# Kernel tuning notes

Hardware: AMD Instinct MI355X
Metric: run time of the kernel (lower is better)

Reference implementation:

```python
import jax, jax.numpy as jnp
import numpy as np

B, T, D, H = 4, 2048, 1024, 16
HD = D // H  # head dim = 64


def setup_inputs() -> dict:
    key = jax.random.key(0)
    ks = jax.random.split(key, 12)
    s = 1.0 / np.sqrt(D)
    inp = {
        "Q": jax.random.normal(ks[0], (B, T, D), jnp.float32),
        "K": jax.random.normal(ks[1], (B, T, D), jnp.float32),
        "V": jax.random.normal(ks[2], (B, T, D), jnp.float32),
        "mask": jnp.tril(jnp.ones((T, T), jnp.int32))[None, None],  # causal [1,1,T,T]
        "Wq": jax.random.normal(ks[3], (D, D), jnp.float32) * s,
        "bq": jax.random.normal(ks[4], (D,), jnp.float32) * s,
        "Wk": jax.random.normal(ks[5], (D, D), jnp.float32) * s,
        "bk": jax.random.normal(ks[6], (D,), jnp.float32) * s,
        "Wv": jax.random.normal(ks[7], (D, D), jnp.float32) * s,
        "bv": jax.random.normal(ks[8], (D,), jnp.float32) * s,
        "Wo": jax.random.normal(ks[9], (D, D), jnp.float32) * s,
        "bo": jax.random.normal(ks[10], (D,), jnp.float32) * s,
    }
    return inp


def reference(Q, K, V, mask, Wq, bq, Wk, bk, Wv, bv, Wo, bo):
    b, t, d = Q.shape
    # projections (torch Linear: x @ W^T + b)
    q = (Q @ Wq.T + bq).reshape(b, t, H, HD).transpose(0, 2, 1, 3)  # [b,h,t,hd]
    k = (K @ Wk.T + bk).reshape(b, t, H, HD).transpose(0, 2, 1, 3)
    v = (V @ Wv.T + bv).reshape(b, t, H, HD).transpose(0, 2, 1, 3)
    score = jnp.einsum("bhqd,bhkd->bhqk", q, k) / jnp.sqrt(jnp.float32(HD))
    score = jnp.where(mask == 0, jnp.float32(-1e9), score)
    attn = jax.nn.softmax(score, axis=-1)
    out = jnp.einsum("bhqk,bhkd->bhqd", attn, v)
    out = out.transpose(0, 2, 1, 3).reshape(b, t, d)
    return out @ Wo.T + bo
```

## Files before the change

kernel.cpp:

```cpp
#include <hip/hip_runtime.h>
#include <stdint.h>

#define B_SZ  4
#define T_SEQ 2048
#define DIM   1024
#define NH    16
#define HD    64
#define M_TOT (B_SZ * T_SEQ)

typedef unsigned short u16;
typedef unsigned long long u64;
typedef __attribute__((ext_vector_type(8))) __bf16 bf16x8;
typedef __attribute__((ext_vector_type(4))) float  floatx4;

#define SCL_Q (0.125f * 1.44269504089f)

__device__ __forceinline__ u16 f2bf(float f) {
  union { float f; uint32_t u; } v; v.f = f;
  uint32_t r = v.u + 0x7fffu + ((v.u >> 16) & 1u);
  return (u16)(r >> 16);
}

__device__ __forceinline__ void gl_lds16(const void* g, void* l) {
  __builtin_amdgcn_global_load_lds(
      (const __attribute__((address_space(1))) uint32_t*)g,
      (__attribute__((address_space(3))) uint32_t*)l, 16, 0, 0);
}

__global__ __launch_bounds__(256) void cvt_all(
    const float* __restrict__ s0, const float* __restrict__ s1,
    const float* __restrict__ s2, const float* __restrict__ s3,
    const float* __restrict__ s4, const float* __restrict__ s5,
    const float* __restrict__ s6,
    u16* __restrict__ d0, u16* __restrict__ d1, u16* __restrict__ d2,
    u16* __restrict__ d3, u16* __restrict__ d4, u16* __restrict__ d5,
    u16* __restrict__ d6) {
  const float* s; u16* d; int n;
  switch (blockIdx.y) {
    case 0: s = s0; d = d0; n = DIM * DIM; break;
    case 1: s = s1; d = d1; n = DIM * DIM; break;
    case 2: s = s2; d = d2; n = DIM * DIM; break;
    case 3: s = s3; d = d3; n = DIM * DIM; break;
    case 4: s = s4; d = d4; n = M_TOT * DIM; break;
    case 5: s = s5; d = d5; n = M_TOT * DIM; break;
    default: s = s6; d = d6; n = M_TOT * DIM; break;
  }
  int i = (blockIdx.x * 256 + threadIdx.x) * 8;
  if (i >= n) return;
  float4 a = *(const float4*)(s + i);
  float4 b = *(const float4*)(s + i + 4);
  uint4 o;
  o.x = (uint32_t)f2bf(a.x) | ((uint32_t)f2bf(a.y) << 16);
  o.y = (uint32_t)f2bf(a.z) | ((uint32_t)f2bf(a.w) << 16);
  o.z = (uint32_t)f2bf(b.x) | ((uint32_t)f2bf(b.y) << 16);
  o.w = (uint32_t)f2bf(b.z) | ((uint32_t)f2bf(b.w) << 16);
  *(uint4*)(d + i) = o;
}

#define BKG 64
__global__ __launch_bounds__(256) void gemm_qkv(
    const u16* __restrict__ Qb, const u16* __restrict__ Kb,
    const u16* __restrict__ Vb,
    const u16* __restrict__ Wq, const u16* __restrict__ Wk,
    const u16* __restrict__ Wv,
    const float* __restrict__ bq, const float* __restrict__ bk,
    const float* __restrict__ bv,
    u16* __restrict__ qo, u16* __restrict__ ko, u16* __restrict__ vo) {
  const u16* A; const u16* Bw; const float* bias; u16* Co;
  if (blockIdx.z == 0)      { A = Qb; Bw = Wq; bias = bq; Co = qo; }
  else if (blockIdx.z == 1) { A = Kb; Bw = Wk; bias = bk; Co = ko; }
  else                      { A = Vb; Bw = Wv; bias = bv; Co = vo; }

  __shared__ u16 As[128 * 64];
  __shared__ u16 Bs[128 * 64];

  const int tid  = threadIdx.x;
  const int wave = tid >> 6, lane = tid & 63;
  const int quad = lane >> 4, l16 = lane & 15;
  const int wm = wave >> 1, wn = wave & 1;
  const int m0 = blockIdx.x * 128, n0 = blockIdx.y * 128;

  const floatx4 FZ = {0.f, 0.f, 0.f, 0.f};
  floatx4 acc[4][4];
#pragma unroll
  for (int mt = 0; mt < 4; ++mt)
#pragma unroll
    for (int nt = 0; nt < 4; ++nt) acc[mt][nt] = FZ;

  for (int k0 = 0; k0 < DIM; k0 += BKG) {
    __syncthreads();
#pragma unroll
    for (int j = 0; j < 4; ++j) {
      int pc = j * 256 + tid;
      int r = pc >> 3, c = pc & 7;
      int sc = c ^ (r & 7);
      gl_lds16(A  + (size_t)(m0 + r) * DIM + k0 + sc * 8,
               &As[(j * 256 + wave * 64) * 8]);
      gl_lds16(Bw + (size_t)(n0 + r) * DIM + k0 + sc * 8,
               &Bs[(j * 256 + wave * 64) * 8]);
    }
    __syncthreads();

#pragma unroll
    for (int kk = 0; kk < 2; ++kk) {
      bf16x8 af[4], bfr[4];
#pragma unroll
      for (int mt = 0; mt < 4; ++mt) {
        int ra = wm * 64 + mt * 16 + l16;
        af[mt] = *(const bf16x8*)&As[ra * 64 + (((kk * 4 + quad) ^ (ra & 7)) * 8)];
      }
#pragma unroll
      for (int nt = 0; nt < 4; ++nt) {
        int rb = wn * 64 + nt * 16 + l16;
        bfr[nt] = *(const bf16x8*)&Bs[rb * 64 + (((kk * 4 + quad) ^ (rb & 7)) * 8)];
      }
#pragma unroll
      for (int mt = 0; mt < 4; ++mt)
#pragma unroll
        for (int nt = 0; nt < 4; ++nt)
          acc[mt][nt] = __builtin_amdgcn_mfma_f32_16x16x32_bf16(
              af[mt], bfr[nt], acc[mt][nt], 0, 0, 0);
    }
  }

  if (blockIdx.z == 2) {
#pragma unroll
    for (int nt = 0; nt < 4; ++nt) {
      int n = n0 + wn * 64 + nt * 16 + l16;
      float bb = bias[n];
      int h = n >> 6, hd = n & 63;
#pragma unroll
      for (int mt = 0; mt < 4; ++mt) {
        int mbase = m0 + wm * 64 + mt * 16 + quad * 4;
        int b = mbase >> 11, t = mbase & (T_SEQ - 1);
        u64 pk = 0;
#pragma unroll
        for (int r = 0; r < 4; ++r)
          pk |= (u64)f2bf(acc[mt][nt][r] + bb) << (16 * r);
        *(u64*)&Co[((size_t)((b * NH + h) * HD + hd)) * T_SEQ + t] = pk;
      }
    }
  } else {
    const float sc = (blockIdx.z == 0) ? SCL_Q : 1.0f;
#pragma unroll
    for (int nt = 0; nt < 4; ++nt) {
      int n = n0 + wn * 64 + nt * 16 + l16;
      float bb = bias[n];
      int h = n >> 6, hd = n & 63;
#pragma unroll
      for (int mt = 0; mt < 4; ++mt) {
#pragma unroll
        for (int r = 0; r < 4; ++r) {
          int m = m0 + wm * 64 + mt * 16 + quad * 4 + r;
          int b = m >> 11, t = m & (T_SEQ - 1);
          Co[((size_t)(b * NH + h) * T_SEQ + t) * HD + hd] =
              f2bf((acc[mt][nt][r] + bb) * sc);
        }
      }
    }
  }
}

__global__ __launch_bounds__(256) void flash_attn(
    const u16* __restrict__ qp, const u16* __restrict__ kp,
    const u16* __restrict__ vp, u16* __restrict__ ao) {
  const int bh = blockIdx.x;
  const int qt = 31 - blockIdx.y;
  const int b = bh >> 4, h = bh & 15;
  const u16* Qg = qp + (size_t)bh * T_SEQ * HD + qt * 64 * HD;
  const u16* Kg = kp + (size_t)bh * T_SEQ * HD;
  const u16* Vg = vp + (size_t)bh * HD * T_SEQ;

  __shared__ u16 lds[4][64 * 64];

  const int tid = threadIdx.x, wave = tid >> 6, lane = tid & 63;
  const int quad = lane >> 4, l16 = lane & 15;
  const int lr8 = lane >> 3, lc8 = lane & 7;

#pragma unroll
  for (int i = 0; i < 2; ++i) {
    int r = i * 32 + wave * 8 + lr8;
    int sc = lc8 ^ (r & 7);
    gl_lds16(Qg + r * 64 + sc * 8, &lds[0][(i * 32 + wave * 8) * 64]);
  }
  __syncthreads();
  bf16x8 bq_[2];
#pragma unroll
  for (int kk = 0; kk < 2; ++kk) {
    int row = wave * 16 + l16;
    int pc = (kk * 4 + quad) ^ (row & 7);
    bq_[kk] = *(const bf16x8*)&lds[0][row * 64 + pc * 8];
  }
  __syncthreads();

  const floatx4 FZ = {0.f, 0.f, 0.f, 0.f};
  floatx4 acco[4];
#pragma unroll
  for (int mt = 0; mt < 4; ++mt) acco[mt] = FZ;
  float l_p = 0.f;

  const int nkb = qt + 1;
  {
#pragma unroll
    for (int i = 0; i < 2; ++i) {
      int r = i * 32 + wave * 8 + lr8;
      int sc = lc8 ^ (r & 7);
      gl_lds16(Kg + r * 64 + sc * 8, &lds[0][(i * 32 + wave * 8) * 64]);
      gl_lds16(Vg + (size_t)r * T_SEQ + sc * 8, &lds[1][(i * 32 + wave * 8) * 64]);
    }
  }

  int p = 0;
  for (int kb = 0; kb < nkb; ++kb) {
    __syncthreads();
    if (kb + 1 < nkb) {
      const u16* Kgk = Kg + (kb + 1) * 64 * HD;
      const u16* Vgk = Vg + (kb + 1) * 64;
#pragma unroll
      for (int i = 0; i < 2; ++i) {
        int r = i * 32 + wave * 8 + lr8;
        int sc = lc8 ^ (r & 7);
        gl_lds16(Kgk + r * 64 + sc * 8, &lds[(p ^ 1) * 2][(i * 32 + wave * 8) * 64]);
        gl_lds16(Vgk + (size_t)r * T_SEQ + sc * 8,
                 &lds[(p ^ 1) * 2 + 1][(i * 32 + wave * 8) * 64]);
      }
    }
    const u16* Ks = &lds[p * 2][0];
    const u16* Vt = &lds[p * 2 + 1][0];

    floatx4 s[4];
#pragma unroll
    for (int mt = 0; mt < 4; ++mt) s[mt] = FZ;
#pragma unroll
    for (int kk = 0; kk < 2; ++kk)
#pragma unroll
      for (int mt = 0; mt < 4; ++mt) {
        int row = mt * 16 + l16;
        bf16x8 ak = *(const bf16x8*)
            &Ks[row * 64 + (((kk * 4 + quad) ^ (l16 & 7)) * 8)];
        s[mt] = __builtin_amdgcn_mfma_f32_16x16x32_bf16(ak, bq_[kk], s[mt], 0, 0, 0);
      }

    if (kb == qt) {
      int qr = wave * 16 + l16;
#pragma unroll
      for (int mt = 0; mt < 4; ++mt)
#pragma unroll
        for (int r = 0; r < 4; ++r) {
          int kvr = mt * 16 + quad * 4 + r;
          if (kvr > qr) s[mt][r] = -3e38f;
        }
    }

    float rs = 0.f;
#pragma unroll
    for (int mt = 0; mt < 4; ++mt)
#pragma unroll
      for (int r = 0; r < 4; ++r) {
        float pv_ = __builtin_amdgcn_exp2f(s[mt][r]);
        s[mt][r] = pv_;
        rs += pv_;
      }
    l_p += rs;

    uint32_t pk[4][2];
#pragma unroll
    for (int mt = 0; mt < 4; ++mt)
#pragma unroll
      for (int hh = 0; hh < 2; ++hh) {
        union { float f; uint32_t u; } a, c;
        a.f = s[mt][2 * hh];
        c.f = s[mt][2 * hh + 1];
        pk[mt][hh] = __builtin_amdgcn_perm(c.u, a.u, 0x07060302);
      }

#pragma unroll
    for (int kkv = 0; kkv < 2; ++kkv) {
      union { uint32_t u[4]; bf16x8 v; } bp;
#pragma unroll
      for (int i = 0; i < 4; ++i) {
        int src = (2 * (quad & 1) + (i >> 1)) * 16 + l16;
        uint32_t v0 = (uint32_t)__shfl((int)pk[kkv * 2][i & 1], src);
        uint32_t v1 = (uint32_t)__shfl((int)pk[kkv * 2 + 1][i & 1], src);
        bp.u[i] = (quad & 2) ? v1 : v0;
      }
#pragma unroll
      for (int mt = 0; mt < 4; ++mt) {
        int row = mt * 16 + l16;
        bf16x8 av = *(const bf16x8*)
            &Vt[row * 64 + (((kkv * 4 + quad) ^ (l16 & 7)) * 8)];
        acco[mt] = __builtin_amdgcn_mfma_f32_16x16x32_bf16(
            av, bp.v, acco[mt], 0, 0, 0);
      }
    }
    p ^= 1;
  }

  {
    float l = l_p;
    l += __shfl_xor(l, 16);
    l += __shfl_xor(l, 32);
    float inv = 1.0f / l;
    int q = qt * 64 + wave * 16 + l16;
#pragma unroll
    for (int mt = 0; mt < 4; ++mt) {
      u64 pkq = 0;
#pragma unroll
      for (int r = 0; r < 4; ++r)
        pkq |= (u64)f2bf(acco[mt][r] * inv) << (16 * r);
      *(u64*)&ao[(size_t)(b * T_SEQ + q) * DIM + h * HD + mt * 16 + quad * 4] = pkq;
    }
  }
}

__global__ __launch_bounds__(256) void gemm_out(
    const u16* __restrict__ Ain, const u16* __restrict__ Wo,
    const float* __restrict__ bo, float* __restrict__ out) {
  __shared__ u16 As[128 * 64];
  __shared__ u16 Bs[128 * 64];

  const int tid  = threadIdx.x;
  const int wave = tid >> 6, lane = tid & 63;
  const int quad = lane >> 4, l16 = lane & 15;
  const int wm = wave >> 1, wn = wave & 1;
  const int m0 = blockIdx.x * 128, n0 = blockIdx.y * 128;

  const floatx4 FZ = {0.f, 0.f, 0.f, 0.f};
  floatx4 acc[4][4];
#pragma unroll
  for (int mt = 0; mt < 4; ++mt)
#pragma unroll
    for (int nt = 0; nt < 4; ++nt) acc[mt][nt] = FZ;

  for (int k0 = 0; k0 < DIM; k0 += BKG) {
    __syncthreads();
#pragma unroll
    for (int j = 0; j < 4; ++j) {
      int pc = j * 256 + tid;
      int r = pc >> 3, c = pc & 7;
      int sc = c ^ (r & 7);
      gl_lds16(Ain + (size_t)(m0 + r) * DIM + k0 + sc * 8,
               &As[(j * 256 + wave * 64) * 8]);
      gl_lds16(Wo  + (size_t)(n0 + r) * DIM + k0 + sc * 8,
               &Bs[(j * 256 + wave * 64) * 8]);
    }
    __syncthreads();

#pragma unroll
    for (int kk = 0; kk < 2; ++kk) {
      bf16x8 af[4], bfr[4];
#pragma unroll
      for (int mt = 0; mt < 4; ++mt) {
        int ra = wm * 64 + mt * 16 + l16;
        af[mt] = *(const bf16x8*)&As[ra * 64 + (((kk * 4 + quad) ^ (ra & 7)) * 8)];
      }
#pragma unroll
      for (int nt = 0; nt < 4; ++nt) {
        int rb = wn * 64 + nt * 16 + l16;
        bfr[nt] = *(const bf16x8*)&Bs[rb * 64 + (((kk * 4 + quad) ^ (rb & 7)) * 8)];
      }
#pragma unroll
      for (int mt = 0; mt < 4; ++mt)
#pragma unroll
        for (int nt = 0; nt < 4; ++nt)
          acc[mt][nt] = __builtin_amdgcn_mfma_f32_16x16x32_bf16(
              af[mt], bfr[nt], acc[mt][nt], 0, 0, 0);
    }
  }

#pragma unroll
  for (int nt = 0; nt < 4; ++nt) {
    int n = n0 + wn * 64 + nt * 16 + l16;
    float bb = bo[n];
#pragma unroll
    for (int mt = 0; mt < 4; ++mt)
#pragma unroll
      for (int r = 0; r < 4; ++r) {
        int m = m0 + wm * 64 + mt * 16 + quad * 4 + r;
        out[(size_t)m * DIM + n] = acc[mt][nt][r] + bb;
      }
  }
}

extern "C" void kernel_launch(void* const* d_in, const int* in_sizes, int n_in,
                              void* d_out, int out_size, void* d_ws,
                              size_t ws_size, hipStream_t stream) {
  const float* Q  = (const float*)d_in[0];
  const float* K  = (const float*)d_in[1];
  const float* V  = (const float*)d_in[2];
  const float* Wq = (const float*)d_in[4];
  const float* bq = (const float*)d_in[5];
  const float* Wk = (const float*)d_in[6];
  const float* bk = (const float*)d_in[7];
  const float* Wv = (const float*)d_in[8];
  const float* bv = (const float*)d_in[9];
  const float* Wo = (const float*)d_in[10];
  const float* bo = (const float*)d_in[11];
  float* out = (float*)d_out;

  u16* wqb = (u16*)d_ws;
  u16* wkb = wqb + 1048576;
  u16* wvb = wkb + 1048576;
  u16* wob = wvb + 1048576;
  u16* Qb  = wob + 1048576;
  u16* Kb  = Qb + (size_t)M_TOT * DIM;
  u16* Vb  = Kb + (size_t)M_TOT * DIM;
  u16* qp  = Vb + (size_t)M_TOT * DIM;
  u16* kp  = qp + (size_t)M_TOT * DIM;
  u16* vp  = kp + (size_t)M_TOT * DIM;
  u16* aop = vp + (size_t)M_TOT * DIM;

  cvt_all<<<dim3(M_TOT * DIM / 2048, 7), 256, 0, stream>>>(
      Wq, Wk, Wv, Wo, Q, K, V, wqb, wkb, wvb, wob, Qb, Kb, Vb);

  gemm_qkv<<<dim3(M_TOT / 128, DIM / 128, 3), 256, 0, stream>>>(
      Qb, Kb, Vb, wqb, wkb, wvb, bq, bk, bv, qp, kp, vp);

  flash_attn<<<dim3(B_SZ * NH, T_SEQ / 64), 256, 0, stream>>>(qp, kp, vp, aop);

  gemm_out<<<dim3(M_TOT / 128, DIM / 128), 256, 0, stream>>>(aop, wob, bo, out);
}
```

Baseline: 324.0 us.

## Use 128-row query tiles with 32x32x16 MFMA in flash attention

The flash attention kernel now handles 128 query rows per block, 32 per wave, instead of 64. It switches from 16x16x32 to 32x32x16 bf16 MFMAs and loads Q fragments straight from global memory into registers. P is rearranged between lanes with permlane32_swap instead of shuffles, and waves skip key blocks that lie fully beyond their causal range. The aim is more reuse of each K/V tile loaded into LDS and fewer shuffle and load instructions, at the cost of fewer blocks and more idle waves inside a block on the diagonal tiles.

New measurement: 316.7 us. 2.3% less time.

```diff
diff --git a/kernel.cpp b/kernel.cpp
--- a/kernel.cpp
+++ b/kernel.cpp
@@ -12,6 +12,7 @@
 typedef unsigned long long u64;
 typedef __attribute__((ext_vector_type(8))) __bf16 bf16x8;
 typedef __attribute__((ext_vector_type(4))) float  floatx4;
+typedef __attribute__((ext_vector_type(16))) float floatx16;
 
 #define SCL_Q (0.125f * 1.44269504089f)
 
@@ -165,150 +166,136 @@
     const u16* __restrict__ qp, const u16* __restrict__ kp,
     const u16* __restrict__ vp, u16* __restrict__ ao) {
   const int bh = blockIdx.x;
-  const int qt = 31 - blockIdx.y;
+  const int qt = (T_SEQ / 128 - 1) - blockIdx.y;
   const int b = bh >> 4, h = bh & 15;
-  const u16* Qg = qp + (size_t)bh * T_SEQ * HD + qt * 64 * HD;
+  const u16* Qg = qp + (size_t)bh * T_SEQ * HD;
   const u16* Kg = kp + (size_t)bh * T_SEQ * HD;
   const u16* Vg = vp + (size_t)bh * HD * T_SEQ;
 
   __shared__ u16 lds[4][64 * 64];
 
   const int tid = threadIdx.x, wave = tid >> 6, lane = tid & 63;
-  const int quad = lane >> 4, l16 = lane & 15;
+  const int hi = lane >> 5, c31 = lane & 31;
   const int lr8 = lane >> 3, lc8 = lane & 7;
+
+  const int qrow = qt * 128 + wave * 32 + c31;
+
+  bf16x8 bq[4];
+#pragma unroll
+  for (int cth = 0; cth < 4; ++cth)
+    bq[cth] = *(const bf16x8*)(Qg + (size_t)qrow * HD + cth * 16 + hi * 8);
+
+  floatx16 o0, o1;
+#pragma unroll
+  for (int i = 0; i < 16; ++i) { o0[i] = 0.f; o1[i] = 0.f; }
+  float l_p = 0.f;
+
+  int koff[4];
+#pragma unroll
+  for (int x = 0; x < 4; ++x)
+    koff[x] = c31 * 64 + (((x * 2 + hi) ^ (c31 & 7)) * 8);
 
 #pragma unroll
   for (int i = 0; i < 2; ++i) {
     int r = i * 32 + wave * 8 + lr8;
     int sc = lc8 ^ (r & 7);
-    gl_lds16(Qg + r * 64 + sc * 8, &lds[0][(i * 32 + wave * 8) * 64]);
-  }
-  __syncthreads();
-  bf16x8 bq_[2];
-#pragma unroll
-  for (int kk = 0; kk < 2; ++kk) {
-    int row = wave * 16 + l16;
-    int pc = (kk * 4 + quad) ^ (row & 7);
-    bq_[kk] = *(const bf16x8*)&lds[0][row * 64 + pc * 8];
-  }
-  __syncthreads();
-
-  const floatx4 FZ = {0.f, 0.f, 0.f, 0.f};
-  floatx4 acco[4];
-#pragma unroll
-  for (int mt = 0; mt < 4; ++mt) acco[mt] = FZ;
-  float l_p = 0.f;
-
-  const int nkb = qt + 1;
-  {
-#pragma unroll
-    for (int i = 0; i < 2; ++i) {
-      int r = i * 32 + wave * 8 + lr8;
-      int sc = lc8 ^ (r & 7);
-      gl_lds16(Kg + r * 64 + sc * 8, &lds[0][(i * 32 + wave * 8) * 64]);
-      gl_lds16(Vg + (size_t)r * T_SEQ + sc * 8, &lds[1][(i * 32 + wave * 8) * 64]);
-    }
-  }
-
+    gl_lds16(Kg + (size_t)r * HD + sc * 8, &lds[0][(i * 32 + wave * 8) * 64]);
+    gl_lds16(Vg + (size_t)r * T_SEQ + sc * 8, &lds[1][(i * 32 + wave * 8) * 64]);
+  }
+
+  const int nkb = 2 * qt + 2;
+  const int qwmin = qt * 128 + wave * 32;
+  const int qwmax = qwmin + 31;
   int p = 0;
   for (int kb = 0; kb < nkb; ++kb) {
     __syncthreads();
     if (kb + 1 < nkb) {
-      const u16* Kgk = Kg + (kb + 1) * 64 * HD;
-      const u16* Vgk = Vg + (kb + 1) * 64;
+      const u16* Kgk = Kg + (size_t)(kb + 1) * 64 * HD;
+      const u16* Vgk = Vg + (size_t)(kb + 1) * 64;
 #pragma unroll
       for (int i = 0; i < 2; ++i) {
         int r = i * 32 + wave * 8 + lr8;
         int sc = lc8 ^ (r & 7);
-        gl_lds16(Kgk + r * 64 + sc * 8, &lds[(p ^ 1) * 2][(i * 32 + wave * 8) * 64]);
+        gl_lds16(Kgk + (size_t)r * HD + sc * 8,
+                 &lds[(p ^ 1) * 2][(i * 32 + wave * 8) * 64]);
         gl_lds16(Vgk + (size_t)r * T_SEQ + sc * 8,
                  &lds[(p ^ 1) * 2 + 1][(i * 32 + wave * 8) * 64]);
       }
     }
-    const u16* Ks = &lds[p * 2][0];
-    const u16* Vt = &lds[p * 2 + 1][0];
-
-    floatx4 s[4];
-#pragma unroll
-    for (int mt = 0; mt < 4; ++mt) s[mt] = FZ;
-#pragma unroll
-    for (int kk = 0; kk < 2; ++kk)
-#pragma unroll
-      for (int mt = 0; mt < 4; ++mt) {
-        int row = mt * 16 + l16;
-        bf16x8 ak = *(const bf16x8*)
-            &Ks[row * 64 + (((kk * 4 + quad) ^ (l16 & 7)) * 8)];
-        s[mt] = __builtin_amdgcn_mfma_f32_16x16x32_bf16(ak, bq_[kk], s[mt], 0, 0, 0);
-      }
-
-    if (kb == qt) {
-      int qr = wave * 16 + l16;
-#pragma unroll
-      for (int mt = 0; mt < 4; ++mt)
-#pragma unroll
-        for (int r = 0; r < 4; ++r) {
-          int kvr = mt * 16 + quad * 4 + r;
-          if (kvr > qr) s[mt][r] = -3e38f;
+
+    if (kb * 64 <= qwmax) {
+      const u16* Ks = &lds[p * 2][0];
+      const u16* Vs = &lds[p * 2 + 1][0];
+
+      floatx16 s0, s1;
+#pragma unroll
+      for (int i = 0; i < 16; ++i) { s0[i] = 0.f; s1[i] = 0.f; }
+#pragma unroll
+      for (int cth = 0; cth < 4; ++cth) {
+        bf16x8 ka = *(const bf16x8*)&Ks[koff[cth]];
+        bf16x8 kb2 = *(const bf16x8*)&Ks[koff[cth] + 32 * 64];
+        s0 = __builtin_amdgcn_mfma_f32_32x32x16_bf16(ka, bq[cth], s0, 0, 0, 0);
+        s1 = __builtin_amdgcn_mfma_f32_32x32x16_bf16(kb2, bq[cth], s1, 0, 0, 0);
+      }
+
+      if (kb * 64 + 63 > qwmin) {
+        int kvb = kb * 64 + 4 * hi;
+#pragma unroll
+        for (int r = 0; r < 16; ++r) {
+          int kvr = kvb + (r & 3) + 8 * (r >> 2);
+          if (kvr > qrow)      s0[r] = -3e38f;
+          if (kvr + 32 > qrow) s1[r] = -3e38f;
         }
-    }
-
-    float rs = 0.f;
-#pragma unroll
-    for (int mt = 0; mt < 4; ++mt)
+      }
+
+      uint32_t pk0[8], pk1[8];
+      float rs = 0.f;
+#pragma unroll
+      for (int rr = 0; rr < 8; ++rr) {
+        union { float f; uint32_t u; } x0, x1, y0, y1;
+        x0.f = __builtin_amdgcn_exp2f(s0[2 * rr]);
+        x1.f = __builtin_amdgcn_exp2f(s0[2 * rr + 1]);
+        y0.f = __builtin_amdgcn_exp2f(s1[2 * rr]);
+        y1.f = __builtin_amdgcn_exp2f(s1[2 * rr + 1]);
+        rs += (x0.f + x1.f) + (y0.f + y1.f);
+        pk0[rr] = __builtin_amdgcn_perm(x1.u, x0.u, 0x07060302);
+        pk1[rr] = __builtin_amdgcn_perm(y1.u, y0.u, 0x07060302);
+      }
+      l_p += rs;
+
+#pragma unroll
+      for (int cc = 0; cc < 4; ++cc) {
+        const uint32_t* pks = (cc & 2) ? pk1 : pk0;
+        const int e4 = (cc & 1) * 4;
+        auto r0 = __builtin_amdgcn_permlane32_swap(pks[e4 + 0], pks[e4 + 2],
+                                                   false, false);
+        auto r1 = __builtin_amdgcn_permlane32_swap(pks[e4 + 1], pks[e4 + 3],
+                                                   false, false);
+        union { uint32_t u[4]; bf16x8 v; } bp;
+        bp.u[0] = r0[0]; bp.u[1] = r1[0]; bp.u[2] = r0[1]; bp.u[3] = r1[1];
+        bf16x8 va = *(const bf16x8*)&Vs[koff[cc]];
+        bf16x8 vb = *(const bf16x8*)&Vs[koff[cc] + 32 * 64];
+        o0 = __builtin_amdgcn_mfma_f32_32x32x16_bf16(va, bp.v, o0, 0, 0, 0);
+        o1 = __builtin_amdgcn_mfma_f32_32x32x16_bf16(vb, bp.v, o1, 0, 0, 0);
+      }
+    }
+    p ^= 1;
+  }
+
+  {
+    float l = l_p + __shfl_xor(l_p, 32);
+    float inv = 1.0f / l;
+    const size_t obase = (size_t)(b * T_SEQ + qrow) * DIM + h * HD;
+#pragma unroll
+    for (int u4 = 0; u4 < 4; ++u4) {
+      u64 w0 = 0, w1 = 0;
 #pragma unroll
       for (int r = 0; r < 4; ++r) {
-        float pv_ = __builtin_amdgcn_exp2f(s[mt][r]);
-        s[mt][r] = pv_;
-        rs += pv_;
-      }
-    l_p += rs;
-
-    uint32_t pk[4][2];
-#pragma unroll
-    for (int mt = 0; mt < 4; ++mt)
-#pragma unroll
-      for (int hh = 0; hh < 2; ++hh) {
-        union { float f; uint32_t u; } a, c;
-        a.f = s[mt][2 * hh];
-        c.f = s[mt][2 * hh + 1];
-        pk[mt][hh] = __builtin_amdgcn_perm(c.u, a.u, 0x07060302);
-      }
-
-#pragma unroll
-    for (int kkv = 0; kkv < 2; ++kkv) {
-      union { uint32_t u[4]; bf16x8 v; } bp;
-#pragma unroll
-      for (int i = 0; i < 4; ++i) {
-        int src = (2 * (quad & 1) + (i >> 1)) * 16 + l16;
-        uint32_t v0 = (uint32_t)__shfl((int)pk[kkv * 2][i & 1], src);
-        uint32_t v1 = (uint32_t)__shfl((int)pk[kkv * 2 + 1][i & 1], src);
-        bp.u[i] = (quad & 2) ? v1 : v0;
-      }
-#pragma unroll
-      for (int mt = 0; mt < 4; ++mt) {
-        int row = mt * 16 + l16;
-        bf16x8 av = *(const bf16x8*)
-            &Vt[row * 64 + (((kkv * 4 + quad) ^ (l16 & 7)) * 8)];
-        acco[mt] = __builtin_amdgcn_mfma_f32_16x16x32_bf16(
-            av, bp.v, acco[mt], 0, 0, 0);
-      }
-    }
-    p ^= 1;
-  }
-
-  {
-    float l = l_p;
-    l += __shfl_xor(l, 16);
-    l += __shfl_xor(l, 32);
-    float inv = 1.0f / l;
-    int q = qt * 64 + wave * 16 + l16;
-#pragma unroll
-    for (int mt = 0; mt < 4; ++mt) {
-      u64 pkq = 0;
-#pragma unroll
-      for (int r = 0; r < 4; ++r)
-        pkq |= (u64)f2bf(acco[mt][r] * inv) << (16 * r);
-      *(u64*)&ao[(size_t)(b * T_SEQ + q) * DIM + h * HD + mt * 16 + quad * 4] = pkq;
+        w0 |= (u64)f2bf(o0[4 * u4 + r] * inv) << (16 * r);
+        w1 |= (u64)f2bf(o1[4 * u4 + r] * inv) << (16 * r);
+      }
+      *(u64*)&ao[obase + 8 * u4 + 4 * hi] = w0;
+      *(u64*)&ao[obase + 32 + 8 * u4 + 4 * hi] = w1;
     }
   }
 }
@@ -416,7 +403,7 @@
   gemm_qkv<<<dim3(M_TOT / 128, DIM / 128, 3), 256, 0, stream>>>(
       Qb, Kb, Vb, wqb, wkb, wvb, bq, bk, bv, qp, kp, vp);
 
-  flash_attn<<<dim3(B_SZ * NH, T_SEQ / 64), 256, 0, stream>>>(qp, kp, vp, aop);
+  flash_attn<<<dim3(B_SZ * NH, T_SEQ / 128), 256, 0, stream>>>(qp, kp, vp, aop);
 
   gemm_out<<<dim3(M_TOT / 128, DIM / 128), 256, 0, stream>>>(aop, wob, bo, out);
 }
```
